# Optimization experiments

Measured on AMD Instinct MI355X. Metric: run time of the kernel, lower is better.

The kernel has to match this reference:

```python
import jax, jax.numpy as jnp
import numpy as np

N_NODES = 5000
N_EDGES = 40000
NUM_ATOM_TYPES = 100
HID = 32            # multiplicity of 0e and 1o in irreps_hidden
EDGE_ATTR_DIM = 8
NUM_BOND_TYPES = 5
OUT_SCALARS = 2 * 6 + 1  # max_charge=6 -> 13x0e
CUTOFF = 5.0
SQRT3 = 1.7320508075688772


def _sh(edge_vec):
    # o3.SphericalHarmonics('1x0e + 1x1o', normalize=True, normalization='component')
    d = jnp.sqrt(jnp.sum(edge_vec * edge_vec, axis=-1) + 1e-12)
    n = edge_vec / d[:, None]
    sh0 = jnp.ones(edge_vec.shape[0], edge_vec.dtype)          # [E]
    sh1 = SQRT3 * n[:, (1, 2, 0)]                              # [E,3], e3nn (y,z,x) order
    return sh0, sh1, d


def _soft_one_hot(d):
    # e3nn.math.soft_one_hot_linspace(d, 0, cutoff, 8, basis='gaussian', cutoff=True)
    values = jnp.linspace(0.0, CUTOFF, EDGE_ATTR_DIM + 2)[1:-1]
    step = CUTOFF / (EDGE_ATTR_DIM + 1)
    diff = (d[:, None] - values[None, :]) / step
    return jnp.exp(-diff * diff) / 1.12


def _mlp(x, W0, b0, W1, b1):
    # ScalarMLP(in, out, hidden=[in], SiLU)
    return jax.nn.silu(x @ W0 + b0) @ W1 + b1


def _tp_init(s, sh0, sh1, w):
    # FCTP(32x0e, 1x0e+1x1o -> 32x0e+32x1o); paths: 0e*0e->0e, 0e*1o->1o
    E = s.shape[0]
    w1 = w[:, : HID * HID].reshape(E, HID, HID)
    w2 = w[:, HID * HID :].reshape(E, HID, HID)
    c = 1.0 / np.sqrt(HID)  # fan-in = 32 per output irrep
    out_s = c * jnp.einsum('eu,euw->ew', s * sh0[:, None], w1)
    out_v = c * jnp.einsum('eu,ei,euw->ewi', s, sh1, w2)
    return out_s, out_v


def _tp_hidden(s, v, sh0, sh1, w):
    # FCTP(32x0e+32x1o, 1x0e+1x1o -> 32x0e+32x1o)
    # path order: 0e*0e->0e, 0e*1o->1o, 1o*0e->1o, 1o*1o->0e
    E = s.shape[0]
    ws = w.reshape(E, 4, HID, HID)
    c = 1.0 / np.sqrt(2 * HID)  # fan-in = 64 per output irrep
    dot = jnp.einsum('eui,ei->eu', v, sh1) / SQRT3  # CG(1,1->0) = delta/sqrt(3)
    out_s = c * (jnp.einsum('eu,euw->ew', s * sh0[:, None], ws[:, 0]) +
                 jnp.einsum('eu,euw->ew', dot, ws[:, 3]))
    out_v = c * (jnp.einsum('eu,ei,euw->ewi', s, sh1, ws[:, 1]) +
                 jnp.einsum('eui,euw->ewi', v * sh0[:, None, None], ws[:, 2]))
    return out_s, out_v


def _edge_tp(s1, v1, s2, v2, sh0, sh1, w):
    # FCTP(64x0e+64x1o (concat of two hidden), 1x0e+1x1o -> 5x0e)
    # blocks in concat order: s_src, v_src, s_dst, v_dst
    E = s1.shape[0]
    ws = w.reshape(E, 4, HID, NUM_BOND_TYPES)
    c = 1.0 / np.sqrt(4 * HID)  # fan-in = 128
    d1 = jnp.einsum('eui,ei->eu', v1, sh1) / SQRT3
    d2 = jnp.einsum('eui,ei->eu', v2, sh1) / SQRT3
    return c * (jnp.einsum('eu,euw->ew', s1 * sh0[:, None], ws[:, 0]) +
                jnp.einsum('eu,euw->ew', d1, ws[:, 1]) +
                jnp.einsum('eu,euw->ew', s2 * sh0[:, None], ws[:, 2]) +
                jnp.einsum('eu,euw->ew', d2, ws[:, 3]))


def _scatter_mean(ms, mv, dst, n):
    cnt = jax.ops.segment_sum(jnp.ones(dst.shape[0], ms.dtype), dst, num_segments=n)
    cnt = jnp.maximum(cnt, 1.0)
    s = jax.ops.segment_sum(ms, dst, num_segments=n) / cnt[:, None]
    v = jax.ops.segment_sum(mv, dst, num_segments=n) / cnt[:, None, None]
    return s, v


def setup_inputs() -> dict:
    key = jax.random.key(0)
    ks = jax.random.split(key, 16)
    def w(k, shape, fan_in):
        return jax.random.normal(k, shape, dtype=jnp.float32) / np.sqrt(fan_in)
    inp = {}
    inp['coordinates'] = jax.random.normal(ks[0], (N_NODES, 3), dtype=jnp.float32) * 1.5
    inp['atom_types'] = jax.random.randint(ks[1], (N_NODES,), 0, NUM_ATOM_TYPES)
    inp['edge_index'] = jax.random.randint(ks[2], (2, N_EDGES), 0, N_NODES)
    inp['atom_embed'] = jax.random.normal(ks[3], (NUM_ATOM_TYPES, HID), dtype=jnp.float32)
    inp['ip_W0'] = w(ks[4], (EDGE_ATTR_DIM, EDGE_ATTR_DIM), EDGE_ATTR_DIM)
    inp['ip_b0'] = jnp.zeros((EDGE_ATTR_DIM,), jnp.float32)
    inp['ip_W1'] = w(ks[5], (EDGE_ATTR_DIM, 2 * HID * HID), EDGE_ATTR_DIM)
    inp['ip_b1'] = jnp.zeros((2 * HID * HID,), jnp.float32)
    inp['ly_W0'] = w(ks[6], (EDGE_ATTR_DIM, EDGE_ATTR_DIM), EDGE_ATTR_DIM)
    inp['ly_b0'] = jnp.zeros((EDGE_ATTR_DIM,), jnp.float32)
    inp['ly_W1'] = w(ks[7], (EDGE_ATTR_DIM, 4 * HID * HID), EDGE_ATTR_DIM)
    inp['ly_b1'] = jnp.zeros((4 * HID * HID,), jnp.float32)
    inp['ly_Ws'] = jax.random.normal(ks[8], (HID, HID), dtype=jnp.float32)
    inp['ly_Wv'] = jax.random.normal(ks[9], (HID, HID), dtype=jnp.float32)
    inp['et_W0'] = w(ks[10], (EDGE_ATTR_DIM, EDGE_ATTR_DIM), EDGE_ATTR_DIM)
    inp['et_b0'] = jnp.zeros((EDGE_ATTR_DIM,), jnp.float32)
    inp['et_W1'] = w(ks[11], (EDGE_ATTR_DIM, 4 * HID * NUM_BOND_TYPES), EDGE_ATTR_DIM)
    inp['et_b1'] = jnp.zeros((4 * HID * NUM_BOND_TYPES,), jnp.float32)
    inp['no_W1'] = jax.random.normal(ks[12], (HID, OUT_SCALARS), dtype=jnp.float32)
    inp['no_W2'] = jax.random.normal(ks[13], (OUT_SCALARS, OUT_SCALARS), dtype=jnp.float32)
    return inp


def reference(coordinates, atom_types, edge_index, atom_embed,
              ip_W0, ip_b0, ip_W1, ip_b1,
              ly_W0, ly_b0, ly_W1, ly_b1, ly_Ws, ly_Wv,
              et_W0, et_b0, et_W1, et_b1, no_W1, no_W2):
    n = coordinates.shape[0]
    src, dst = edge_index[0], edge_index[1]
    edge_vec = coordinates[dst] - coordinates[src]
    sh0, sh1, d = _sh(edge_vec)
    edge_attr = _soft_one_hot(d)                              # [E,8]
    # initial projector: Conv(32x0e -> 32x0e+32x1o)
    s0 = atom_embed[atom_types]                               # [N,32]
    w_ip = _mlp(edge_attr, ip_W0, ip_b0, ip_W1, ip_b1)        # [E,2048]
    ms, mv = _tp_init(s0[src], sh0, sh1, w_ip)
    s, v = _scatter_mean(ms, mv, dst, n)                      # [N,32],[N,32,3]
    # one LinearSelfInteraction(Conv) layer
    w_ly = _mlp(edge_attr, ly_W0, ly_b0, ly_W1, ly_b1)        # [E,4096]
    ms, mv = _tp_hidden(s[src], v[src], sh0, sh1, w_ly)
    cs, cv = _scatter_mean(ms, mv, dst, n)
    lc = 1.0 / np.sqrt(HID)  # e3nn o3.Linear normalization
    s = cs + lc * (s @ ly_Ws)
    v = cv + lc * jnp.einsum('eui,uw->ewi', v, ly_Wv)
    # edge output: FCTP([h_src, h_dst], edge_sh) with radial weights
    w_et = _mlp(edge_attr, et_W0, et_b0, et_W1, et_b1)        # [E,640]
    edge_out = _edge_tp(s[src], v[src], s[dst], v[dst], sh0, sh1, w_et)  # [E,5]
    # node output MLP on detached scalar channel (13x0e)
    sd = jax.lax.stop_gradient(s)
    h = jax.nn.silu(sd @ no_W1 / np.sqrt(HID))
    node_out = h @ no_W2 / np.sqrt(OUT_SCALARS)               # [N,13]
    return edge_out, node_out
```

## Files before the change

### kernel.cpp

```cpp
#include <hip/hip_runtime.h>

#define NN 5000
#define NE 40000

typedef unsigned int u32;
typedef unsigned short u16;
typedef __fp16 h16x2 __attribute__((ext_vector_type(2)));
typedef _Float16 f16x8 __attribute__((ext_vector_type(8)));
typedef __attribute__((ext_vector_type(4))) float f32x4;

union AF { u32 u[4]; f16x8 v; uint4 q; };

__device__ __forceinline__ float siluf(float x) { return x / (1.f + __expf(-x)); }

__device__ __forceinline__ u32 f2bf_u(float f) {
  u32 x = __float_as_uint(f);
  return (x + 0x7FFFu + ((x >> 16) & 1u)) >> 16;
}
__device__ __forceinline__ u32 packbf2(float lo, float hi) {
  return f2bf_u(lo) | (f2bf_u(hi) << 16);
}
__device__ __forceinline__ u32 pkh2(float a, float b) {
  union { h16x2 h; u32 u; } r;
  r.h = __builtin_amdgcn_cvt_pkrtz(a, b);
  return r.u;
}
__device__ __forceinline__ u16 f2h(float v) {
  _Float16 h = (_Float16)v;
  return *(u16*)&h;
}
__device__ __forceinline__ void unpack8(uint4 q, float* f) {
  f[0] = __uint_as_float(q.x << 16); f[1] = __uint_as_float(q.x & 0xFFFF0000u);
  f[2] = __uint_as_float(q.y << 16); f[3] = __uint_as_float(q.y & 0xFFFF0000u);
  f[4] = __uint_as_float(q.z << 16); f[5] = __uint_as_float(q.z & 0xFFFF0000u);
  f[6] = __uint_as_float(q.w << 16); f[7] = __uint_as_float(q.w & 0xFFFF0000u);
}
__device__ __forceinline__ float dot8f(const float* h, const float* w, float init) {
  float a = init;
#pragma unroll
  for (int k = 0; k < 8; k++) a = fmaf(h[k], w[k], a);
  return a;
}
__device__ __forceinline__ void mlp8(const float* ea, const float* __restrict__ W0,
                                     const float* __restrict__ b0, float* h) {
#pragma unroll
  for (int j = 0; j < 8; j++) {
    float a = b0[j];
#pragma unroll
    for (int i = 0; i < 8; i++) a += ea[i] * W0[i*8 + j];
    h[j] = siluf(a);
  }
}
__device__ __forceinline__ AF mkfrag(float hs, const float* s) {
  AF a;
  a.u[0] = pkh2(hs*s[0], hs*s[1]);
  a.u[1] = pkh2(hs*s[2], hs*s[3]);
  a.u[2] = pkh2(hs*s[4], hs*s[5]);
  a.u[3] = pkh2(hs*s[6], hs*s[7]);
  return a;
}
__device__ __forceinline__ float bf2f(u16 v) { return __uint_as_float(((u32)v) << 16); }

__global__ __launch_bounds__(256) void k_conv1(
    const float* __restrict__ coords, const int* __restrict__ eidx,
    const float* __restrict__ emb, const int* __restrict__ atype,
    const float* __restrict__ ipW0, const float* __restrict__ ipb0,
    const float* __restrict__ lyW0, const float* __restrict__ lyb0,
    const float* __restrict__ etW0, const float* __restrict__ etb0,
    const float* __restrict__ ipW1, const float* __restrict__ ipb1,
    float* __restrict__ sh, float* __restrict__ h_ly, float* __restrict__ h_et,
    int* __restrict__ cur, int* __restrict__ slot, u16* __restrict__ msg) {
  __shared__ __align__(16) u16 B2[18432];
  {
    int col = threadIdx.x & 63, pth = col >> 5, w = col & 31;
    int k0 = (threadIdx.x >> 6) * 72;
    for (int k = k0; k < k0 + 72; k++) {
      float v = (k < 256) ? ipW1[(k >> 5)*2048 + pth*1024 + (k & 31)*32 + w]
                          : ipb1[pth*1024 + (k - 256)*32 + w];
      B2[((k >> 3)*64 + col)*8 + (k & 7)] = f2h(v);
    }
  }
  int wid = threadIdx.x >> 6, lane = threadIdx.x & 63;
  int tile = blockIdx.x*4 + wid;
  int m = lane & 15, q = lane >> 4;
  int e = tile*16 + m;
  int s = eidx[e], d = eidx[NE + e];
  float vx = coords[d*3+0] - coords[s*3+0];
  float vy = coords[d*3+1] - coords[s*3+1];
  float vz = coords[d*3+2] - coords[s*3+2];
  float dist = sqrtf(vx*vx + vy*vy + vz*vz + 1e-12f);
  float dinv = 1.f / dist;
  const float SQ3 = 1.7320508075688772f;
  float sh0 = SQ3 * vy * dinv;
  float sh1 = SQ3 * vz * dinv;
  float sh2 = SQ3 * vx * dinv;
  int srow = atype[s];
  float ea[8];
  const float step = 5.f / 9.f;
#pragma unroll
  for (int jj = 0; jj < 8; jj++) {
    float diff = (dist - step * (float)(jj+1)) * (9.f / 5.f);
    ea[jj] = __expf(-diff*diff) * (1.f / 1.12f);
  }
  float hip[8], hly[8], het[8];
  mlp8(ea, ipW0, ipb0, hip);
  mlp8(ea, lyW0, lyb0, hly);
  mlp8(ea, etW0, etb0, het);
  int t = 0;
  if (q == 0) {
    sh[e*3+0] = sh0; sh[e*3+1] = sh1; sh[e*3+2] = sh2;
    { float4 f0 = {hly[0],hly[1],hly[2],hly[3]}, f1 = {hly[4],hly[5],hly[6],hly[7]};
      *(float4*)&h_ly[e*8] = f0; *(float4*)&h_ly[e*8+4] = f1; }
    { float4 f0 = {het[0],het[1],het[2],het[3]}, f1 = {het[4],het[5],het[6],het[7]};
      *(float4*)&h_et[e*8] = f0; *(float4*)&h_et[e*8+4] = f1; }
    int* cp = &cur[d];
    atomicCAS(cp, (int)0xAAAAAAAA, 0);
    t = atomicAdd(cp, 1);
    slot[e] = t;
  }
  float4 sA = *(const float4*)&emb[srow*32 + q*8];
  float4 sB = *(const float4*)&emb[srow*32 + q*8 + 4];
  float sf[8] = {sA.x,sA.y,sA.z,sA.w,sB.x,sB.y,sB.z,sB.w};
  __syncthreads();
  f32x4 acc0 = {0.f,0.f,0.f,0.f}, acc1 = acc0, acc2 = acc0, acc3 = acc0;
  const float cs = 0.17677669529663687f;
#pragma unroll
  for (int ks = 0; ks < 9; ks++) {
    float hs = (ks < 8) ? hip[ks] : 1.f;
    AF a = mkfrag(hs, sf);
    int c2 = (ks*4 + q)*64;
    AF b0, b1f, b2, b3;
    b0.q  = *(const uint4*)&B2[(c2 +  0 + m)*8];
    b1f.q = *(const uint4*)&B2[(c2 + 16 + m)*8];
    b2.q  = *(const uint4*)&B2[(c2 + 32 + m)*8];
    b3.q  = *(const uint4*)&B2[(c2 + 48 + m)*8];
    acc0 = __builtin_amdgcn_mfma_f32_16x16x32_f16(a.v, b0.v,  acc0, 0, 0, 0);
    acc1 = __builtin_amdgcn_mfma_f32_16x16x32_f16(a.v, b1f.v, acc1, 0, 0, 0);
    acc2 = __builtin_amdgcn_mfma_f32_16x16x32_f16(a.v, b2.v,  acc2, 0, 0, 0);
    acc3 = __builtin_amdgcn_mfma_f32_16x16x32_f16(a.v, b3.v,  acc3, 0, 0, 0);
  }
#pragma unroll
  for (int r = 0; r < 4; r++) {
    int L = q*4 + r;
    int tE = __shfl(t, L, 64);
    int dn = __shfl(d, L, 64);
    float s0v = __shfl(sh0, L, 64);
    float s1v = __shfl(sh1, L, 64);
    float s2v = __shfl(sh2, L, 64);
    if (tE < 64) {
      u16* mp = msg + ((size_t)dn*64 + tE)*128;
      float m0 = cs*acc2[r], m1 = cs*acc3[r];
      uint2 p0 = { packbf2(cs*acc0[r], m0*s0v), packbf2(m0*s1v, m0*s2v) };
      *(uint2*)&mp[m*4] = p0;
      uint2 p1 = { packbf2(cs*acc1[r], m1*s0v), packbf2(m1*s1v, m1*s2v) };
      *(uint2*)&mp[64 + m*4] = p1;
    }
  }
}

__global__ __launch_bounds__(256) void k_gather1(
    const u16* __restrict__ msg, const int* __restrict__ cur,
    float* __restrict__ s1, float* __restrict__ v1soa) {
  int ln = threadIdx.x >> 7, c = threadIdx.x & 127;
  int n = blockIdx.x*2 + ln;
  int deg = min(cur[n], 64);
  const u16* base = msg + (size_t)n*64*128 + c;
  float acc = 0.f;
  int j = 0;
  for (; j + 4 <= deg; j += 4) {
    float x0 = bf2f(base[(j+0)*128]);
    float x1 = bf2f(base[(j+1)*128]);
    float x2 = bf2f(base[(j+2)*128]);
    float x3 = bf2f(base[(j+3)*128]);
    acc += (x0 + x1) + (x2 + x3);
  }
  for (; j < deg; j++) acc += bf2f(base[j*128]);
  acc /= (float)max(deg, 1);
  int col = c >> 2, comp = c & 3;
  if (comp == 0) s1[n*32 + col] = acc;
  else           v1soa[(comp-1)*160000 + n*32 + col] = acc;
}

__global__ __launch_bounds__(256) void k_conv2(
    const float* __restrict__ hE, const float* __restrict__ sh,
    const float* __restrict__ s1, const float* __restrict__ v1soa,
    const int* __restrict__ eidx, const int* __restrict__ slot,
    const float* __restrict__ lyW1, const float* __restrict__ lyb1,
    u16* __restrict__ msgA, u16* __restrict__ msgB) {
  __shared__ __align__(16) u16 B2[18432];
  const bool scalarHalf = blockIdx.x < 625;
  int blk = scalarHalf ? blockIdx.x : blockIdx.x - 625;
  {
    int col = threadIdx.x & 63;
    int k0 = (threadIdx.x >> 6) * 72;
    int basec = scalarHalf ? ((col >> 5)*1024 + (col & 31))
                           : ((col < 32) ? (2048 + col) : (3072 + (col - 32)));
    for (int k = k0; k < k0 + 72; k++) {
      float v = (k < 256) ? lyW1[(k >> 5)*4096 + basec + (k & 31)*32]
                          : lyb1[basec + (k - 256)*32];
      B2[((k >> 3)*64 + col)*8 + (k & 7)] = f2h(v);
    }
  }
  int wid = threadIdx.x >> 6, lane = threadIdx.x & 63;
  int tile = blk*4 + wid;
  int m = lane & 15, q = lane >> 4;
  const float c = 0.125f;
  int e = tile*16 + m;
  int srcn = eidx[e];
  int dnv  = eidx[NE + e];
  int slv  = slot[e];
  float s0p = sh[e*3+0], s1p = sh[e*3+1], s2p = sh[e*3+2];
  float4 hA = *(const float4*)&hE[e*8];
  float4 hB = *(const float4*)&hE[e*8 + 4];
  float hf[8] = {hA.x,hA.y,hA.z,hA.w,hB.x,hB.y,hB.z,hB.w};
  __syncthreads();

  if (scalarHalf) {
    float4 sA = *(const float4*)&s1[srcn*32 + q*8];
    float4 sB = *(const float4*)&s1[srcn*32 + q*8 + 4];
    float sf[8] = {sA.x,sA.y,sA.z,sA.w,sB.x,sB.y,sB.z,sB.w};
    f32x4 acc0 = {0.f,0.f,0.f,0.f}, acc1 = acc0, acc2 = acc0, acc3 = acc0;
#pragma unroll
    for (int ks = 0; ks < 9; ks++) {
      float hs = (ks < 8) ? hf[ks] : 1.f;
      AF a = mkfrag(hs, sf);
      int c2 = (ks*4 + q)*64;
      AF b0, b1f, b2, b3;
      b0.q  = *(const uint4*)&B2[(c2 +  0 + m)*8];
      b1f.q = *(const uint4*)&B2[(c2 + 16 + m)*8];
      b2.q  = *(const uint4*)&B2[(c2 + 32 + m)*8];
      b3.q  = *(const uint4*)&B2[(c2 + 48 + m)*8];
      acc0 = __builtin_amdgcn_mfma_f32_16x16x32_f16(a.v, b0.v,  acc0, 0, 0, 0);
      acc1 = __builtin_amdgcn_mfma_f32_16x16x32_f16(a.v, b1f.v, acc1, 0, 0, 0);
      acc2 = __builtin_amdgcn_mfma_f32_16x16x32_f16(a.v, b2.v,  acc2, 0, 0, 0);
      acc3 = __builtin_amdgcn_mfma_f32_16x16x32_f16(a.v, b3.v,  acc3, 0, 0, 0);
    }
#pragma unroll
    for (int r = 0; r < 4; r++) {
      int L = q*4 + r;
      int tE = __shfl(slv, L, 64);
      int dn = __shfl(dnv, L, 64);
      float s0v = __shfl(s0p, L, 64);
      float s1v = __shfl(s1p, L, 64);
      float s2v = __shfl(s2p, L, 64);
      if (tE < 64) {
        u16* mp = msgA + ((size_t)dn*64 + tE)*128;
        float m0 = c*acc2[r], m1 = c*acc3[r];
        uint2 p0 = { packbf2(c*acc0[r], m0*s0v), packbf2(m0*s1v, m0*s2v) };
        *(uint2*)&mp[m*4] = p0;
        uint2 p1 = { packbf2(c*acc1[r], m1*s0v), packbf2(m1*s1v, m1*s2v) };
        *(uint2*)&mp[64 + m*4] = p1;
      }
    }
  } else {
    const float is3 = 0.5773502691896258f;
    float vf[3][8];
#pragma unroll
    for (int i = 0; i < 3; i++) {
      float4 aa = *(const float4*)&v1soa[i*160000 + srcn*32 + q*8];
      float4 bb = *(const float4*)&v1soa[i*160000 + srcn*32 + q*8 + 4];
      vf[i][0]=aa.x; vf[i][1]=aa.y; vf[i][2]=aa.z; vf[i][3]=aa.w;
      vf[i][4]=bb.x; vf[i][5]=bb.y; vf[i][6]=bb.z; vf[i][7]=bb.w;
    }
    float df[8];
#pragma unroll
    for (int j = 0; j < 8; j++)
      df[j] = (vf[0][j]*s0p + vf[1][j]*s1p + vf[2][j]*s2p) * is3;
    f32x4 z = {0.f,0.f,0.f,0.f};
    f32x4 aV00 = z, aV01 = z, aV10 = z, aV11 = z, aV20 = z, aV21 = z, aD0 = z, aD1 = z;
#pragma unroll
    for (int ks = 0; ks < 9; ks++) {
      float hs = (ks < 8) ? hf[ks] : 1.f;
      int c2 = (ks*4 + q)*64;
      AF b0, b1f, b2, b3;
      b0.q  = *(const uint4*)&B2[(c2 +  0 + m)*8];
      b1f.q = *(const uint4*)&B2[(c2 + 16 + m)*8];
      b2.q  = *(const uint4*)&B2[(c2 + 32 + m)*8];
      b3.q  = *(const uint4*)&B2[(c2 + 48 + m)*8];
      AF a0 = mkfrag(hs, vf[0]);
      AF a1 = mkfrag(hs, vf[1]);
      AF a2 = mkfrag(hs, vf[2]);
      AF ad = mkfrag(hs, df);
      aV00 = __builtin_amdgcn_mfma_f32_16x16x32_f16(a0.v, b0.v,  aV00, 0, 0, 0);
      aV01 = __builtin_amdgcn_mfma_f32_16x16x32_f16(a0.v, b1f.v, aV01, 0, 0, 0);
      aV10 = __builtin_amdgcn_mfma_f32_16x16x32_f16(a1.v, b0.v,  aV10, 0, 0, 0);
      aV11 = __builtin_amdgcn_mfma_f32_16x16x32_f16(a1.v, b1f.v, aV11, 0, 0, 0);
      aV20 = __builtin_amdgcn_mfma_f32_16x16x32_f16(a2.v, b0.v,  aV20, 0, 0, 0);
      aV21 = __builtin_amdgcn_mfma_f32_16x16x32_f16(a2.v, b1f.v, aV21, 0, 0, 0);
      aD0  = __builtin_amdgcn_mfma_f32_16x16x32_f16(ad.v, b2.v,  aD0,  0, 0, 0);
      aD1  = __builtin_amdgcn_mfma_f32_16x16x32_f16(ad.v, b3.v,  aD1,  0, 0, 0);
    }
#pragma unroll
    for (int r = 0; r < 4; r++) {
      int L = q*4 + r;
      int tE = __shfl(slv, L, 64);
      int dn = __shfl(dnv, L, 64);
      if (tE < 64) {
        u16* mp = msgB + ((size_t)dn*64 + tE)*128;
        uint2 p0 = { packbf2(c*aD0[r], c*aV00[r]), packbf2(c*aV10[r], c*aV20[r]) };
        *(uint2*)&mp[m*4] = p0;
        uint2 p1 = { packbf2(c*aD1[r], c*aV01[r]), packbf2(c*aV11[r], c*aV21[r]) };
        *(uint2*)&mp[64 + m*4] = p1;
      }
    }
  }
}

__global__ __launch_bounds__(256) void k_gather2(
    const u16* __restrict__ msgA, const u16* __restrict__ msgB,
    const int* __restrict__ cur,
    const float* __restrict__ s1, const float* __restrict__ v1soa,
    const float* __restrict__ Ws, const float* __restrict__ Wv,
    const float* __restrict__ noW1, const float* __restrict__ noW2,
    float* __restrict__ s2, float* __restrict__ v2, float* __restrict__ outN) {
  __shared__ float sb[2][32];
  __shared__ float hb[2][13];
  int ln = threadIdx.x >> 7, c = threadIdx.x & 127;
  int n = blockIdx.x*2 + ln;
  int deg = min(cur[n], 64);
  const u16* bA = msgA + (size_t)n*64*128 + c;
  const u16* bB = msgB + (size_t)n*64*128 + c;
  float acc = 0.f;
  int j = 0;
  for (; j + 4 <= deg; j += 4) {
    float x0 = bf2f(bA[(j+0)*128]) + bf2f(bB[(j+0)*128]);
    float x1 = bf2f(bA[(j+1)*128]) + bf2f(bB[(j+1)*128]);
    float x2 = bf2f(bA[(j+2)*128]) + bf2f(bB[(j+2)*128]);
    float x3 = bf2f(bA[(j+3)*128]) + bf2f(bB[(j+3)*128]);
    acc += (x0 + x1) + (x2 + x3);
  }
  for (; j < deg; j++) acc += bf2f(bA[j*128]) + bf2f(bB[j*128]);
  acc /= (float)max(deg, 1);
  const float lc = 0.17677669529663687f;
  int col = c >> 2, comp = c & 3;
  if (comp == 0) {
    float ss = 0.f;
#pragma unroll 8
    for (int u = 0; u < 32; u++) ss += s1[n*32 + u] * Ws[u*32 + col];
    float val = acc + lc*ss;
    s2[n*32 + col] = val;
    sb[ln][col] = val;
  } else {
    int i = comp - 1;
    float sv = 0.f;
#pragma unroll 8
    for (int u = 0; u < 32; u++) sv += v1soa[i*160000 + n*32 + u] * Wv[u*32 + col];
    v2[n*96 + col*3 + i] = acc + lc*sv;
  }
  __syncthreads();
  const float i32 = 0.17677669529663687f;
  if (c < 13) {
    float a = 0.f;
#pragma unroll 8
    for (int u = 0; u < 32; u++) a += sb[ln][u] * noW1[u*13 + c];
    hb[ln][c] = siluf(a * i32);
  }
  __syncthreads();
  const float i13 = 0.2773500981126146f;
  if (c < 13) {
    float a = 0.f;
#pragma unroll
    for (int j2 = 0; j2 < 13; j2++) a += hb[ln][j2] * noW2[j2*13 + c];
    outN[n*13 + c] = a * i13;
  }
}

__global__ __launch_bounds__(256) void k_e3(
    const float* __restrict__ hE, const float* __restrict__ sh,
    const float* __restrict__ s2, const float* __restrict__ v2,
    const int* __restrict__ eidx,
    const float* __restrict__ W1, const float* __restrict__ b1,
    float* __restrict__ out) {
  __shared__ uint4 WQ[640];
  __shared__ float BQ[640];
  for (int t = threadIdx.x; t < 640; t += 256) {
    int u = t & 31, pw = t >> 5, p2 = pw / 5, w = pw - p2*5;
    int col = p2*160 + u*5 + w;
    const float* s = W1 + col;
    uint4 q;
    q.x = packbf2(s[0],      s[640]);
    q.y = packbf2(s[1280],   s[1920]);
    q.z = packbf2(s[2560],   s[3200]);
    q.w = packbf2(s[3840],   s[4480]);
    WQ[t] = q;
    BQ[t] = b1[col];
  }
  __syncthreads();
  const int g = threadIdx.x >> 5, tw = threadIdx.x & 31;
  const float c = 0.08838834764831845f;
  const float is3 = 0.5773502691896258f;
  for (int p = blockIdx.x*8 + g; p*2 < NE; p += gridDim.x*8) {
    int e0 = p*2, e1 = e0 + 1;
    float h0[8], h1[8];
    {
      float4 qa = *(const float4*)&hE[e0*8];
      float4 qb = *(const float4*)&hE[e0*8+4];
      h0[0]=qa.x; h0[1]=qa.y; h0[2]=qa.z; h0[3]=qa.w;
      h0[4]=qb.x; h0[5]=qb.y; h0[6]=qb.z; h0[7]=qb.w;
      float4 qc = *(const float4*)&hE[e1*8];
      float4 qd = *(const float4*)&hE[e1*8+4];
      h1[0]=qc.x; h1[1]=qc.y; h1[2]=qc.z; h1[3]=qc.w;
      h1[4]=qd.x; h1[5]=qd.y; h1[6]=qd.z; h1[7]=qd.w;
    }
    int sA = eidx[e0], dA = eidx[NE+e0];
    int sB = eidx[e1], dB = eidx[NE+e1];
    float sa0 = sh[e0*3+0], sa1 = sh[e0*3+1], sa2 = sh[e0*3+2];
    float sb0 = sh[e1*3+0], sb1 = sh[e1*3+1], sb2 = sh[e1*3+2];
    float c00 = s2[sA*32 + tw];
    float c01 = (v2[sA*96+tw*3+0]*sa0 + v2[sA*96+tw*3+1]*sa1 + v2[sA*96+tw*3+2]*sa2) * is3;
    float c02 = s2[dA*32 + tw];
    float c03 = (v2[dA*96+tw*3+0]*sa0 + v2[dA*96+tw*3+1]*sa1 + v2[dA*96+tw*3+2]*sa2) * is3;
    float c10 = s2[sB*32 + tw];
    float c11 = (v2[sB*96+tw*3+0]*sb0 + v2[sB*96+tw*3+1]*sb1 + v2[sB*96+tw*3+2]*sb2) * is3;
    float c12 = s2[dB*32 + tw];
    float c13 = (v2[dB*96+tw*3+0]*sb0 + v2[dB*96+tw*3+1]*sb1 + v2[dB*96+tw*3+2]*sb2) * is3;
    float part0[5] = {0,0,0,0,0};
    float part1[5] = {0,0,0,0,0};
#pragma unroll
    for (int pp = 0; pp < 4; pp++) {
      float cp0 = (pp==0) ? c00 : (pp==1) ? c01 : (pp==2) ? c02 : c03;
      float cp1 = (pp==0) ? c10 : (pp==1) ? c11 : (pp==2) ? c12 : c13;
#pragma unroll
      for (int w = 0; w < 5; w++) {
        int idx = (pp*5 + w)*32 + tw;
        float f[8];
        unpack8(WQ[idx], f);
        float bv = BQ[idx];
        part0[w] = fmaf(cp0, dot8f(h0, f, bv), part0[w]);
        part1[w] = fmaf(cp1, dot8f(h1, f, bv), part1[w]);
      }
    }
#pragma unroll
    for (int off = 16; off > 0; off >>= 1)
#pragma unroll
      for (int w = 0; w < 5; w++) {
        part0[w] += __shfl_xor(part0[w], off, 32);
        part1[w] += __shfl_xor(part1[w], off, 32);
      }
    float outv = 0.f;
#pragma unroll
    for (int w = 0; w < 5; w++) {
      if (tw == w)     outv = part0[w];
      if (tw == 5 + w) outv = part1[w];
    }
    if (tw < 10) out[e0*5 + tw] = c * outv;
  }
}

extern "C" void kernel_launch(void* const* d_in, const int* in_sizes, int n_in,
                              void* d_out, int out_size, void* d_ws, size_t ws_size,
                              hipStream_t stream) {
  (void)in_sizes; (void)n_in; (void)out_size; (void)ws_size;
  const float* coords = (const float*)d_in[0];
  const int*   atype  = (const int*)d_in[1];
  const int*   eidx   = (const int*)d_in[2];
  const float* emb    = (const float*)d_in[3];
  const float* ipW0 = (const float*)d_in[4];
  const float* ipb0 = (const float*)d_in[5];
  const float* ipW1 = (const float*)d_in[6];
  const float* ipb1 = (const float*)d_in[7];
  const float* lyW0 = (const float*)d_in[8];
  const float* lyb0 = (const float*)d_in[9];
  const float* lyW1 = (const float*)d_in[10];
  const float* lyb1 = (const float*)d_in[11];
  const float* lyWs = (const float*)d_in[12];
  const float* lyWv = (const float*)d_in[13];
  const float* etW0 = (const float*)d_in[14];
  const float* etb0 = (const float*)d_in[15];
  const float* etW1 = (const float*)d_in[16];
  const float* etb1 = (const float*)d_in[17];
  const float* noW1 = (const float*)d_in[18];
  const float* noW2 = (const float*)d_in[19];

  float* ws = (float*)d_ws;
  float* sh    = ws;
  float* h_ly  = ws + 120000;
  float* h_et  = ws + 440000;
  float* s1    = ws + 760000;
  float* v1soa = ws + 920000;
  float* s2    = ws + 1400000;
  float* v2    = ws + 1560000;
  int*   cur   = (int*)(ws + 2040000);
  int*   slot  = (int*)(ws + 2045000);
  u16*   msgA  = (u16*)(ws + 2085000);
  u16*   msgB  = (u16*)(ws + 22565000);

  float* outE = (float*)d_out;
  float* outN = (float*)d_out + NE*5;

  k_conv1<<<625, 256, 0, stream>>>(coords, eidx, emb, atype,
                                   ipW0, ipb0, lyW0, lyb0, etW0, etb0,
                                   ipW1, ipb1, sh, h_ly, h_et, cur, slot, msgA);
  k_gather1<<<NN/2, 256, 0, stream>>>(msgA, cur, s1, v1soa);
  k_conv2<<<1250, 256, 0, stream>>>(h_ly, sh, s1, v1soa, eidx, slot,
                                    lyW1, lyb1, msgA, msgB);
  k_gather2<<<NN/2, 256, 0, stream>>>(msgA, msgB, cur, s1, v1soa,
                                      lyWs, lyWv, noW1, noW2, s2, v2, outN);
  k_e3<<<1024, 256, 0, stream>>>(h_et, sh, s2, v2, eidx, etW1, etb1, outE);
}
```

Baseline: 182.0 us.

## Pre-pack fp16 weight tiles once in a prep kernel, read B from global

```diff
diff --git a/kernel.cpp b/kernel.cpp
--- a/kernel.cpp
+++ b/kernel.cpp
@@ -61,25 +61,51 @@
 }
 __device__ __forceinline__ float bf2f(u16 v) { return __uint_as_float(((u32)v) << 16); }
 
+__global__ __launch_bounds__(256) void k_prep(
+    const float* __restrict__ ipW1, const float* __restrict__ ipb1,
+    const float* __restrict__ lyW1, const float* __restrict__ lyb1,
+    u16* __restrict__ ipT, u16* __restrict__ lyT) {
+  int b = blockIdx.x;
+  if (b < 16) {
+    int h = b >> 3;
+    int t0 = (b & 7)*2304 + threadIdx.x*9;
+#pragma unroll
+    for (int j = 0; j < 9; j++) {
+      int t = t0 + j;
+      int kch = t >> 9, rem = t & 511;
+      int col = rem >> 3, kk = rem & 7;
+      int k = kch*8 + kk;
+      int basec = (h == 0) ? ((col >> 5)*1024 + (col & 31))
+                           : ((col < 32) ? (2048 + col) : (3072 + (col - 32)));
+      float v = (k < 256) ? lyW1[(k >> 5)*4096 + basec + (k & 31)*32]
+                          : lyb1[basec + (k - 256)*32];
+      lyT[h*18432 + t] = f2h(v);
+    }
+  } else {
+    int t0 = (b - 16)*2304 + threadIdx.x*9;
+#pragma unroll
+    for (int j = 0; j < 9; j++) {
+      int t = t0 + j;
+      int kch = t >> 9, rem = t & 511;
+      int col = rem >> 3, kk = rem & 7;
+      int k = kch*8 + kk;
+      int pth = col >> 5, w = col & 31;
+      float v = (k < 256) ? ipW1[(k >> 5)*2048 + pth*1024 + (k & 31)*32 + w]
+                          : ipb1[pth*1024 + (k - 256)*32 + w];
+      ipT[t] = f2h(v);
+    }
+  }
+}
+
 __global__ __launch_bounds__(256) void k_conv1(
     const float* __restrict__ coords, const int* __restrict__ eidx,
     const float* __restrict__ emb, const int* __restrict__ atype,
     const float* __restrict__ ipW0, const float* __restrict__ ipb0,
     const float* __restrict__ lyW0, const float* __restrict__ lyb0,
     const float* __restrict__ etW0, const float* __restrict__ etb0,
-    const float* __restrict__ ipW1, const float* __restrict__ ipb1,
+    const u16* __restrict__ ipT,
     float* __restrict__ sh, float* __restrict__ h_ly, float* __restrict__ h_et,
     int* __restrict__ cur, int* __restrict__ slot, u16* __restrict__ msg) {
-  __shared__ __align__(16) u16 B2[18432];
-  {
-    int col = threadIdx.x & 63, pth = col >> 5, w = col & 31;
-    int k0 = (threadIdx.x >> 6) * 72;
-    for (int k = k0; k < k0 + 72; k++) {
-      float v = (k < 256) ? ipW1[(k >> 5)*2048 + pth*1024 + (k & 31)*32 + w]
-                          : ipb1[pth*1024 + (k - 256)*32 + w];
-      B2[((k >> 3)*64 + col)*8 + (k & 7)] = f2h(v);
-    }
-  }
   int wid = threadIdx.x >> 6, lane = threadIdx.x & 63;
   int tile = blockIdx.x*4 + wid;
   int m = lane & 15, q = lane >> 4;
@@ -121,7 +147,6 @@
   float4 sA = *(const float4*)&emb[srow*32 + q*8];
   float4 sB = *(const float4*)&emb[srow*32 + q*8 + 4];
   float sf[8] = {sA.x,sA.y,sA.z,sA.w,sB.x,sB.y,sB.z,sB.w};
-  __syncthreads();
   f32x4 acc0 = {0.f,0.f,0.f,0.f}, acc1 = acc0, acc2 = acc0, acc3 = acc0;
   const float cs = 0.17677669529663687f;
 #pragma unroll
@@ -130,10 +155,10 @@
     AF a = mkfrag(hs, sf);
     int c2 = (ks*4 + q)*64;
     AF b0, b1f, b2, b3;
-    b0.q  = *(const uint4*)&B2[(c2 +  0 + m)*8];
-    b1f.q = *(const uint4*)&B2[(c2 + 16 + m)*8];
-    b2.q  = *(const uint4*)&B2[(c2 + 32 + m)*8];
-    b3.q  = *(const uint4*)&B2[(c2 + 48 + m)*8];
+    b0.q  = *(const uint4*)&ipT[(c2 +  0 + m)*8];
+    b1f.q = *(const uint4*)&ipT[(c2 + 16 + m)*8];
+    b2.q  = *(const uint4*)&ipT[(c2 + 32 + m)*8];
+    b3.q  = *(const uint4*)&ipT[(c2 + 48 + m)*8];
     acc0 = __builtin_amdgcn_mfma_f32_16x16x32_f16(a.v, b0.v,  acc0, 0, 0, 0);
     acc1 = __builtin_amdgcn_mfma_f32_16x16x32_f16(a.v, b1f.v, acc1, 0, 0, 0);
     acc2 = __builtin_amdgcn_mfma_f32_16x16x32_f16(a.v, b2.v,  acc2, 0, 0, 0);
@@ -185,25 +210,14 @@
     const float* __restrict__ hE, const float* __restrict__ sh,
     const float* __restrict__ s1, const float* __restrict__ v1soa,
     const int* __restrict__ eidx, const int* __restrict__ slot,
-    const float* __restrict__ lyW1, const float* __restrict__ lyb1,
+    const u16* __restrict__ lyT,
     u16* __restrict__ msgA, u16* __restrict__ msgB) {
-  __shared__ __align__(16) u16 B2[18432];
+  int wid = threadIdx.x >> 6, lane = threadIdx.x & 63;
   const bool scalarHalf = blockIdx.x < 625;
   int blk = scalarHalf ? blockIdx.x : blockIdx.x - 625;
-  {
-    int col = threadIdx.x & 63;
-    int k0 = (threadIdx.x >> 6) * 72;
-    int basec = scalarHalf ? ((col >> 5)*1024 + (col & 31))
-                           : ((col < 32) ? (2048 + col) : (3072 + (col - 32)));
-    for (int k = k0; k < k0 + 72; k++) {
-      float v = (k < 256) ? lyW1[(k >> 5)*4096 + basec + (k & 31)*32]
-                          : lyb1[basec + (k - 256)*32];
-      B2[((k >> 3)*64 + col)*8 + (k & 7)] = f2h(v);
-    }
-  }
-  int wid = threadIdx.x >> 6, lane = threadIdx.x & 63;
   int tile = blk*4 + wid;
   int m = lane & 15, q = lane >> 4;
+  const u16* Bg = lyT + (scalarHalf ? 0 : 18432);
   const float c = 0.125f;
   int e = tile*16 + m;
   int srcn = eidx[e];
@@ -213,7 +227,6 @@
   float4 hA = *(const float4*)&hE[e*8];
   float4 hB = *(const float4*)&hE[e*8 + 4];
   float hf[8] = {hA.x,hA.y,hA.z,hA.w,hB.x,hB.y,hB.z,hB.w};
-  __syncthreads();
 
   if (scalarHalf) {
     float4 sA = *(const float4*)&s1[srcn*32 + q*8];
@@ -226,10 +239,10 @@
       AF a = mkfrag(hs, sf);
       int c2 = (ks*4 + q)*64;
       AF b0, b1f, b2, b3;
-      b0.q  = *(const uint4*)&B2[(c2 +  0 + m)*8];
-      b1f.q = *(const uint4*)&B2[(c2 + 16 + m)*8];
-      b2.q  = *(const uint4*)&B2[(c2 + 32 + m)*8];
-      b3.q  = *(const uint4*)&B2[(c2 + 48 + m)*8];
+      b0.q  = *(const uint4*)&Bg[(c2 +  0 + m)*8];
+      b1f.q = *(const uint4*)&Bg[(c2 + 16 + m)*8];
+      b2.q  = *(const uint4*)&Bg[(c2 + 32 + m)*8];
+      b3.q  = *(const uint4*)&Bg[(c2 + 48 + m)*8];
       acc0 = __builtin_amdgcn_mfma_f32_16x16x32_f16(a.v, b0.v,  acc0, 0, 0, 0);
       acc1 = __builtin_amdgcn_mfma_f32_16x16x32_f16(a.v, b1f.v, acc1, 0, 0, 0);
       acc2 = __builtin_amdgcn_mfma_f32_16x16x32_f16(a.v, b2.v,  acc2, 0, 0, 0);
@@ -273,10 +286,10 @@
       float hs = (ks < 8) ? hf[ks] : 1.f;
       int c2 = (ks*4 + q)*64;
       AF b0, b1f, b2, b3;
-      b0.q  = *(const uint4*)&B2[(c2 +  0 + m)*8];
-      b1f.q = *(const uint4*)&B2[(c2 + 16 + m)*8];
-      b2.q  = *(const uint4*)&B2[(c2 + 32 + m)*8];
-      b3.q  = *(const uint4*)&B2[(c2 + 48 + m)*8];
+      b0.q  = *(const uint4*)&Bg[(c2 +  0 + m)*8];
+      b1f.q = *(const uint4*)&Bg[(c2 + 16 + m)*8];
+      b2.q  = *(const uint4*)&Bg[(c2 + 32 + m)*8];
+      b3.q  = *(const uint4*)&Bg[(c2 + 48 + m)*8];
       AF a0 = mkfrag(hs, vf[0]);
       AF a1 = mkfrag(hs, vf[1]);
       AF a2 = mkfrag(hs, vf[2]);
@@ -484,16 +497,19 @@
   int*   slot  = (int*)(ws + 2045000);
   u16*   msgA  = (u16*)(ws + 2085000);
   u16*   msgB  = (u16*)(ws + 22565000);
+  u16*   lyT   = (u16*)(ws + 43045000);
+  u16*   ipT   = (u16*)(ws + 43063432);
 
   float* outE = (float*)d_out;
   float* outN = (float*)d_out + NE*5;
 
+  k_prep<<<24, 256, 0, stream>>>(ipW1, ipb1, lyW1, lyb1, ipT, lyT);
   k_conv1<<<625, 256, 0, stream>>>(coords, eidx, emb, atype,
                                    ipW0, ipb0, lyW0, lyb0, etW0, etb0,
-                                   ipW1, ipb1, sh, h_ly, h_et, cur, slot, msgA);
+                                   ipT, sh, h_ly, h_et, cur, slot, msgA);
   k_gather1<<<NN/2, 256, 0, stream>>>(msgA, cur, s1, v1soa);
   k_conv2<<<1250, 256, 0, stream>>>(h_ly, sh, s1, v1soa, eidx, slot,
-                                    lyW1, lyb1, msgA, msgB);
+                                    lyT, msgA, msgB);
   k_gather2<<<NN/2, 256, 0, stream>>>(msgA, msgB, cur, s1, v1soa,
                                       lyWs, lyWv, noW1, noW2, s2, v2, outN);
   k_e3<<<1024, 256, 0, stream>>>(h_et, sh, s2, v2, eidx, etW1, etb1, outE);
```

New measurement: 168.1 us. 1.08x faster.
